# Optimization experiments

Hardware: AMD Instinct MI355X
Metric: run time of the kernel (lower is better)

Reference implementation:

```python
import jax, jax.numpy as jnp
import numpy as np

A_MIN = 0.5
A_MAX = 5.0


def setup_inputs() -> dict:
    key = jax.random.key(0)
    k1, k2 = jax.random.split(key)
    S = jax.random.uniform(k1, (32, 1024, 1024), dtype=jnp.float32)  # [B,H,W] in [0,1]
    u_i = jax.random.normal(k2, (16,), dtype=jnp.float32)
    return {"S": S, "u_i": u_i, "M": 16}


def reference(S, u_i, M):
    # slopes per segment: a_min + (a_max - a_min) * sigmoid(u_i)
    a_i = A_MIN + (A_MAX - A_MIN) * jax.nn.sigmoid(u_i)  # [M]
    delta = 1.0 / M
    bounds = jnp.linspace(0.0, 1.0, M + 1, dtype=S.dtype)  # [M+1]
    Y = jnp.sum(a_i) * delta  # total mapped length
    # torch.bucketize(S, bounds, right=True) == searchsorted(bounds, S, side='right')
    j = jnp.clip(jnp.searchsorted(bounds, S, side="right") - 1, 0, M - 1)  # [B,H,W]
    # cumulative length before segment j: tiny cumsum + per-pixel gather
    # (replaces the original O(M) full-tensor loop)
    cum = jnp.concatenate([jnp.zeros((1,), dtype=S.dtype), jnp.cumsum(a_i * delta)])  # [M+1]
    S_total = cum[j] + a_i[j] * (S - bounds[j])
    return S_total / Y
```

## Files before the change

kernel.cpp:

```cpp
#include <hip/hip_runtime.h>


typedef float vf4 __attribute__((ext_vector_type(4)));

#define MSEG 16
#define VPT  8
#define BLK  256

__global__ __launch_bounds__(BLK) void mapping_kernel(
    const vf4* __restrict__ S4,
    const float* __restrict__ u,
    vf4* __restrict__ out4,
    int n4)
{
    __shared__ float sA[MSEG];
    __shared__ float sB[MSEG];

    const int tid = threadIdx.x;

    if (tid < 64) {
        float a = 0.0f;
        if (tid < MSEG) {
            float sig = 1.0f / (1.0f + expf(-u[tid]));
            a = 0.5f + 4.5f * sig;
        }
        float p = a;
        #pragma unroll
        for (int off = 1; off < MSEG; off <<= 1) {
            float t = __shfl_up(p, off, 64);
            if (tid >= off) p += t;
        }
        float total = __shfl(p, MSEG - 1, 64);
        if (tid < MSEG) {
            float invY = 16.0f / total;
            float cum  = (p - a) * (1.0f / 16.0f);
            sA[tid] = a * invY;
            sB[tid] = (cum - a * ((float)tid * (1.0f / 16.0f))) * invY;
        }
    }
    __syncthreads();

    const int base = blockIdx.x * (BLK * VPT) + tid;

    if (base + (VPT - 1) * BLK < n4) {
        vf4 v[VPT];
        #pragma unroll
        for (int k = 0; k < VPT; ++k)
            v[k] = __builtin_nontemporal_load(&S4[base + k * BLK]);

        __builtin_amdgcn_sched_barrier(0);

        #pragma unroll
        for (int k = 0; k < VPT; ++k) {
            const vf4 s = v[k];
            vf4 r;
            const int jx = min(max((int)(s.x * 16.0f), 0), 15);
            const int jy = min(max((int)(s.y * 16.0f), 0), 15);
            const int jz = min(max((int)(s.z * 16.0f), 0), 15);
            const int jw = min(max((int)(s.w * 16.0f), 0), 15);
            r.x = fmaf(s.x, sA[jx], sB[jx]);
            r.y = fmaf(s.y, sA[jy], sB[jy]);
            r.z = fmaf(s.z, sA[jz], sB[jz]);
            r.w = fmaf(s.w, sA[jw], sB[jw]);
            __builtin_nontemporal_store(r, &out4[base + k * BLK]);
        }
    } else {
        #pragma unroll
        for (int k = 0; k < VPT; ++k) {
            const int i = base + k * BLK;
            if (i < n4) {
                const vf4 s = __builtin_nontemporal_load(&S4[i]);
                vf4 r;
                const int jx = min(max((int)(s.x * 16.0f), 0), 15);
                const int jy = min(max((int)(s.y * 16.0f), 0), 15);
                const int jz = min(max((int)(s.z * 16.0f), 0), 15);
                const int jw = min(max((int)(s.w * 16.0f), 0), 15);
                r.x = fmaf(s.x, sA[jx], sB[jx]);
                r.y = fmaf(s.y, sA[jy], sB[jy]);
                r.z = fmaf(s.z, sA[jz], sB[jz]);
                r.w = fmaf(s.w, sA[jw], sB[jw]);
                __builtin_nontemporal_store(r, &out4[i]);
            }
        }
    }
}

extern "C" void kernel_launch(void* const* d_in, const int* in_sizes, int n_in,
                              void* d_out, int out_size, void* d_ws, size_t ws_size,
                              hipStream_t stream)
{
    const vf4*  S4 = (const vf4*)d_in[0];
    const float* u = (const float*)d_in[1];

    vf4* out4 = (vf4*)d_out;
    const int n4 = out_size / 4;

    const int grid = (n4 + BLK * VPT - 1) / (BLK * VPT);
    mapping_kernel<<<grid, BLK, 0, stream>>>(S4, u, out4, n4);
}
```

Measured before the change: 221.5 us.

## Use persistent grid-stride blocks with double-buffered register prefetch

Launches at most 1024 blocks that loop over chunks in grid-stride order. Each block loads the next chunk into a second register buffer while computing and storing the current one. The per-block segment-table setup is amortized over several chunks. The cost is higher register pressure and fewer resident waves, which may reduce memory-level parallelism.

```diff
diff --git a/kernel.cpp b/kernel.cpp
--- a/kernel.cpp
+++ b/kernel.cpp
@@ -6,6 +6,35 @@
 #define MSEG 16
 #define VPT  8
 #define BLK  256
+#define NBLOCKS 1024
+
+#define CHUNK (BLK * VPT)
+
+__device__ __forceinline__ void load_chunk(vf4 (&v)[VPT], const vf4* __restrict__ S4, int base)
+{
+    #pragma unroll
+    for (int k = 0; k < VPT; ++k)
+        v[k] = __builtin_nontemporal_load(&S4[base + k * BLK]);
+}
+
+__device__ __forceinline__ void compute_store(const vf4 (&v)[VPT], vf4* __restrict__ out4,
+                                              int base, const float* sA, const float* sB)
+{
+    #pragma unroll
+    for (int k = 0; k < VPT; ++k) {
+        const vf4 s = v[k];
+        vf4 r;
+        const int jx = min(max((int)(s.x * 16.0f), 0), 15);
+        const int jy = min(max((int)(s.y * 16.0f), 0), 15);
+        const int jz = min(max((int)(s.z * 16.0f), 0), 15);
+        const int jw = min(max((int)(s.w * 16.0f), 0), 15);
+        r.x = fmaf(s.x, sA[jx], sB[jx]);
+        r.y = fmaf(s.y, sA[jy], sB[jy]);
+        r.z = fmaf(s.z, sA[jz], sB[jz]);
+        r.w = fmaf(s.w, sA[jw], sB[jw]);
+        __builtin_nontemporal_store(r, &out4[base + k * BLK]);
+    }
+}
 
 __global__ __launch_bounds__(BLK) void mapping_kernel(
     const vf4* __restrict__ S4,
@@ -40,19 +69,12 @@
     }
     __syncthreads();
 
-    const int base = blockIdx.x * (BLK * VPT) + tid;
+    const int nfull  = n4 / CHUNK;
+    const int stride = gridDim.x;
 
-    if (base + (VPT - 1) * BLK < n4) {
-        vf4 v[VPT];
-        #pragma unroll
-        for (int k = 0; k < VPT; ++k)
-            v[k] = __builtin_nontemporal_load(&S4[base + k * BLK]);
-
-        __builtin_amdgcn_sched_barrier(0);
-
-        #pragma unroll
-        for (int k = 0; k < VPT; ++k) {
-            const vf4 s = v[k];
+    if (blockIdx.x == 0) {
+        for (int i = nfull * CHUNK + tid; i < n4; i += BLK) {
+            const vf4 s = __builtin_nontemporal_load(&S4[i]);
             vf4 r;
             const int jx = min(max((int)(s.x * 16.0f), 0), 15);
             const int jy = min(max((int)(s.y * 16.0f), 0), 15);
@@ -62,26 +84,32 @@
             r.y = fmaf(s.y, sA[jy], sB[jy]);
             r.z = fmaf(s.z, sA[jz], sB[jz]);
             r.w = fmaf(s.w, sA[jw], sB[jw]);
-            __builtin_nontemporal_store(r, &out4[base + k * BLK]);
+            __builtin_nontemporal_store(r, &out4[i]);
         }
-    } else {
-        #pragma unroll
-        for (int k = 0; k < VPT; ++k) {
-            const int i = base + k * BLK;
-            if (i < n4) {
-                const vf4 s = __builtin_nontemporal_load(&S4[i]);
-                vf4 r;
-                const int jx = min(max((int)(s.x * 16.0f), 0), 15);
-                const int jy = min(max((int)(s.y * 16.0f), 0), 15);
-                const int jz = min(max((int)(s.z * 16.0f), 0), 15);
-                const int jw = min(max((int)(s.w * 16.0f), 0), 15);
-                r.x = fmaf(s.x, sA[jx], sB[jx]);
-                r.y = fmaf(s.y, sA[jy], sB[jy]);
-                r.z = fmaf(s.z, sA[jz], sB[jz]);
-                r.w = fmaf(s.w, sA[jw], sB[jw]);
-                __builtin_nontemporal_store(r, &out4[i]);
-            }
-        }
+    }
+
+    int c = blockIdx.x;
+    if (c >= nfull) return;
+
+    vf4 vA[VPT], vB[VPT];
+    load_chunk(vA, S4, c * CHUNK + tid);
+
+    for (;;) {
+        int c1 = c + stride;
+        bool more1 = (c1 < nfull);
+        if (more1) load_chunk(vB, S4, c1 * CHUNK + tid);
+        __builtin_amdgcn_sched_barrier(0);
+        compute_store(vA, out4, c * CHUNK + tid, sA, sB);
+        if (!more1) break;
+
+        int c2 = c1 + stride;
+        bool more2 = (c2 < nfull);
+        if (more2) load_chunk(vA, S4, c2 * CHUNK + tid);
+        __builtin_amdgcn_sched_barrier(0);
+        compute_store(vB, out4, c1 * CHUNK + tid, sA, sB);
+        if (!more2) break;
+
+        c = c2;
     }
 }
 
@@ -95,6 +123,7 @@
     vf4* out4 = (vf4*)d_out;
     const int n4 = out_size / 4;
 
-    const int grid = (n4 + BLK * VPT - 1) / (BLK * VPT);
+    const int nchunk = (n4 + CHUNK - 1) / CHUNK;
+    const int grid = nchunk < NBLOCKS ? (nchunk > 0 ? nchunk : 1) : NBLOCKS;
     mapping_kernel<<<grid, BLK, 0, stream>>>(S4, u, out4, n4);
 }
```

After: 224.4 us. Within noise of the previous version (+1.3%).
